# Kernel optimization log

Measured on AMD Instinct MI355X. Metric: run time of the kernel, lower is better.

## Reference

```python
import jax, jax.numpy as jnp
import numpy as np
import math

N = 50000          # nodes
E = 800000         # edges (~avg degree 16)
G = 2048           # graphs
NUM_RBF = 128
CUTOFF = 5.0       # max_radius
C_RAD = 16         # radial channels
SH_DIM = 9         # 1x0e+1x1e+1x2e
_AVG_DEGREE = 15.57930850982666
_AVG_NUM_NODES = 18.03065905448718


def spherical_harmonics_l012(vec):
    """e3nn spherical harmonics l=0,1,2, normalize=True, component normalization."""
    r = jnp.linalg.norm(vec, axis=-1, keepdims=True)
    u = vec / jnp.maximum(r, 1e-12)
    x, y, z = u[..., 0], u[..., 1], u[..., 2]
    s3, s5, s15 = math.sqrt(3.0), math.sqrt(5.0), math.sqrt(15.0)
    x2, y2, z2 = x * x, y * y, z * z
    return jnp.stack([
        jnp.ones_like(x),                 # l=0
        s3 * x, s3 * y, s3 * z,           # l=1
        s15 * x * z,                      # l=2 (e3nn ordering)
        s15 * x * y,
        s5 * (y2 - 0.5 * (x2 + z2)),
        s15 * y * z,
        (s15 / 2.0) * (z2 - x2),
    ], axis=-1)


def exp_normal_smearing(dist):
    """ExpNormalSmearing with cutoff_lower=0, cutoff_upper=CUTOFF, num_rbf=NUM_RBF."""
    alpha = 5.0 / CUTOFF
    start = math.exp(-CUTOFF)
    means = jnp.linspace(start, 1.0, NUM_RBF).astype(dist.dtype)
    beta = (2.0 / NUM_RBF * (1.0 - start)) ** (-2)
    d = dist[..., None]
    cut = 0.5 * (jnp.cos(d * math.pi / CUTOFF) + 1.0) * (d < CUTOFF).astype(d.dtype)
    return cut * jnp.exp(-beta * (jnp.exp(-alpha * d) - means) ** 2)


def setup_inputs() -> dict:
    key = jax.random.key(0)
    ks = jax.random.split(key, 16)
    s = 0.05
    return {
        "pos": jax.random.normal(ks[0], (N, 3), jnp.float32) * 2.0,
        "atom_table": jax.random.normal(ks[1], (64, C_RAD * SH_DIM), jnp.float32) * s,
        "W1": jax.random.normal(ks[2], (NUM_RBF, 64), jnp.float32) * s,
        "b1": jnp.zeros((64,), jnp.float32),
        "W2": jax.random.normal(ks[3], (64, 64), jnp.float32) * s,
        "b2": jnp.zeros((64,), jnp.float32),
        "W3": jax.random.normal(ks[4], (64, C_RAD), jnp.float32) * s,
        "Wh1": jax.random.normal(ks[5], (C_RAD * SH_DIM, C_RAD * SH_DIM), jnp.float32) * s,
        "bh1": jnp.zeros((C_RAD * SH_DIM,), jnp.float32),
        "Wh2": jax.random.normal(ks[6], (C_RAD * SH_DIM, 1), jnp.float32) * s,
        "bh2": jnp.zeros((1,), jnp.float32),
        "node_atom": jax.random.randint(ks[7], (N,), 0, 64, jnp.int32),
        "edge_src": jax.random.randint(ks[8], (E,), 0, N, jnp.int32),
        "edge_dst": jax.random.randint(ks[9], (E,), 0, N, jnp.int32),
        "batch": jnp.sort(jax.random.randint(ks[10], (N,), 0, G, jnp.int32)),
    }


def reference(pos, atom_table, W1, b1, W2, b2, W3, Wh1, bh1, Wh2, bh2,
              node_atom, edge_src, edge_dst, batch):
    # edge geometry
    edge_vec = pos[edge_src] - pos[edge_dst]                      # [E,3]
    edge_len = jnp.linalg.norm(edge_vec, axis=-1)                 # [E]
    rbf = exp_normal_smearing(edge_len)                           # [E,128]
    sh = spherical_harmonics_l012(edge_vec)                       # [E,9]

    # radial MLP (fc_neurons = [128,64,64] -> C_RAD weights)
    h = jax.nn.silu(rbf @ W1 + b1)
    h = jax.nn.silu(h @ W2 + b2)
    rad = h @ W3                                                  # [E,C_RAD]

    # RBF-conditioned tensor-product-style edge message: outer(radial, sh)
    msg = (rad[:, :, None] * sh[:, None, :]).reshape(rad.shape[0], C_RAD * SH_DIM)

    # scatter-add aggregation, rescaled by avg degree (EdgeDegreeEmbedding)
    deg_embed = jax.ops.segment_sum(msg, edge_dst, num_segments=N)
    deg_embed = deg_embed / math.sqrt(_AVG_DEGREE)                # [N,144]

    node_features = atom_table[node_atom] + deg_embed             # [N,144]

    # energy head: Linear -> SiLU -> Linear(1x0e)
    hn = jax.nn.silu(node_features @ Wh1 + bh1)
    node_energy = hn @ Wh2 + bh2                                  # [N,1]

    # ScaledScatter over graphs
    energy = jax.ops.segment_sum(node_energy, batch, num_segments=G)
    energy = energy / math.sqrt(_AVG_NUM_NODES)                   # [G,1]
    return energy
```

## Files before the change

### kernel.cpp

```cpp
#include <hip/hip_runtime.h>
#include <math.h>

#define NND 50000
#define NED 800000
#define NGR 2048
#define NT  1024
#define NB  512
#define NPB 98
#define HALF 49
#define BCAP 2048
#define SCAP 1152
#define LCAP 24
#define LSTR 25
#define BIN_BLOCKS 196
#define TBL_BLOCKS 2

constexpr double dSTART = 0.006737946999085467;
constexpr float  K_START = (float)dSTART;
constexpr float  K_STEP  = (float)((1.0 - dSTART) / 127.0);
constexpr float  K_BETA  = (float)(1.0 / ((2.0/128.0*(1.0-dSTART)) * (2.0/128.0*(1.0-dSTART))));
constexpr float  K_TSTEP = (float)((1.0 - dSTART) / (double)(NT - 1));
constexpr float  K_INVT  = (float)((double)(NT - 1) / (1.0 - dSTART));

__device__ __forceinline__ float silu_f(float x) {
    return x * __builtin_amdgcn_rcpf(1.0f + __expf(-x));
}

__global__ void __launch_bounds__(1024)
bin_table(const int* __restrict__ esrc, const int* __restrict__ edst,
          int* __restrict__ bincnt, unsigned* __restrict__ bins,
          const float* __restrict__ W1, const float* __restrict__ b1,
          const float* __restrict__ W2, const float* __restrict__ b2,
          const float* __restrict__ W3, float* __restrict__ table,
          float* __restrict__ out)
{
    __shared__ unsigned smem[NB + NB * LSTR];
    const int bid = blockIdx.x;
    const int tid = threadIdx.x;

    if (bid < BIN_BLOCKS) {
        int*      lcnt = (int*)smem;
        unsigned* lbuf = smem + NB;
        if (tid < NB) lcnt[tid] = 0;
        __syncthreads();
        const int e0 = bid * 4096;
        #pragma unroll
        for (int r = 0; r < 4; ++r) {
            int e = e0 + r * 1024 + tid;
            if (e < NED) {
                int dst = edst[e];
                int src = esrc[e];
                int b = dst / NPB;
                unsigned rec = ((unsigned)src << 7) | (unsigned)(dst - b * NPB);
                int p = atomicAdd(&lcnt[b], 1);
                if (p < LCAP) lbuf[b * LSTR + p] = rec;
                else {
                    int gp = atomicAdd(&bincnt[b], 1);
                    if (gp < BCAP) bins[b * BCAP + gp] = rec;
                }
            }
        }
        __syncthreads();
        if (tid < NB) {
            int c = lcnt[tid]; c = c < LCAP ? c : LCAP;
            if (c > 0) {
                int base = atomicAdd(&bincnt[tid], c);
                for (int i = 0; i < c; ++i)
                    if (base + i < BCAP) bins[tid * BCAP + base + i] = lbuf[tid * LSTR + i];
            }
        }
        return;
    }

    const int tb = bid - BIN_BLOCKS;
    out[tb * 1024 + tid] = 0.0f;
    if (tid >= 512) return;
    const int ti = tb * 512 + tid;
    const int l  = tid & 63;
    float* hb = (float*)smem + (tid >> 6) * (64 * 17);

    const float xe = K_START + K_TSTEP * (float)ti;
    const float dd = -logf(xe);
    const float cutv = (dd < 5.0f) ? (0.5f * (__cosf(dd * 0.6283185307179586f) + 1.0f)) : 0.0f;

    float h1[64];
    {
        const float4* bp = (const float4*)b1;
        #pragma unroll
        for (int j4 = 0; j4 < 16; ++j4) {
            float4 b = bp[j4];
            h1[4*j4+0] = b.x; h1[4*j4+1] = b.y; h1[4*j4+2] = b.z; h1[4*j4+3] = b.w;
        }
    }
    #pragma unroll 2
    for (int k = 0; k < 128; ++k) {
        float mean = K_START + K_STEP * (float)k;
        float t = xe - mean;
        float rk = cutv * __expf(-K_BETA * t * t);
        const float4* wr = (const float4*)(W1 + (k << 6));
        #pragma unroll
        for (int j4 = 0; j4 < 16; ++j4) {
            float4 wv = wr[j4];
            h1[4*j4+0] = fmaf(rk, wv.x, h1[4*j4+0]);
            h1[4*j4+1] = fmaf(rk, wv.y, h1[4*j4+1]);
            h1[4*j4+2] = fmaf(rk, wv.z, h1[4*j4+2]);
            h1[4*j4+3] = fmaf(rk, wv.w, h1[4*j4+3]);
        }
    }

    float h2[64];
    {
        const float4* bp = (const float4*)b2;
        #pragma unroll
        for (int j4 = 0; j4 < 16; ++j4) {
            float4 b = bp[j4];
            h2[4*j4+0] = b.x; h2[4*j4+1] = b.y; h2[4*j4+2] = b.z; h2[4*j4+3] = b.w;
        }
    }
    #pragma unroll
    for (int ch = 0; ch < 4; ++ch) {
        #pragma unroll
        for (int j = 0; j < 16; ++j) hb[l*17 + j] = silu_f(h1[ch*16 + j]);
        for (int k = 0; k < 16; ++k) {
            float hk = hb[l*17 + k];
            const float4* wr = (const float4*)(W2 + ((ch*16 + k) << 6));
            #pragma unroll
            for (int j4 = 0; j4 < 16; ++j4) {
                float4 wv = wr[j4];
                h2[4*j4+0] = fmaf(hk, wv.x, h2[4*j4+0]);
                h2[4*j4+1] = fmaf(hk, wv.y, h2[4*j4+1]);
                h2[4*j4+2] = fmaf(hk, wv.z, h2[4*j4+2]);
                h2[4*j4+3] = fmaf(hk, wv.w, h2[4*j4+3]);
            }
        }
    }

    float rad[16];
    #pragma unroll
    for (int cc = 0; cc < 16; ++cc) rad[cc] = 0.0f;
    #pragma unroll
    for (int ch = 0; ch < 4; ++ch) {
        #pragma unroll
        for (int j = 0; j < 16; ++j) hb[l*17 + j] = silu_f(h2[ch*16 + j]);
        for (int k = 0; k < 16; ++k) {
            float hk = hb[l*17 + k];
            const float4* wr = (const float4*)(W3 + ((ch*16 + k) << 4));
            #pragma unroll
            for (int c4 = 0; c4 < 4; ++c4) {
                float4 wv = wr[c4];
                rad[4*c4+0] = fmaf(hk, wv.x, rad[4*c4+0]);
                rad[4*c4+1] = fmaf(hk, wv.y, rad[4*c4+1]);
                rad[4*c4+2] = fmaf(hk, wv.z, rad[4*c4+2]);
                rad[4*c4+3] = fmaf(hk, wv.w, rad[4*c4+3]);
            }
        }
    }

    float4* rp = (float4*)(table + (size_t)ti * 16);
    rp[0] = make_float4(rad[0],  rad[1],  rad[2],  rad[3]);
    rp[1] = make_float4(rad[4],  rad[5],  rad[6],  rad[7]);
    rp[2] = make_float4(rad[8],  rad[9],  rad[10], rad[11]);
    rp[3] = make_float4(rad[12], rad[13], rad[14], rad[15]);
}

__global__ void __launch_bounds__(448)
agg_head(const float* __restrict__ pos,
         const int* __restrict__ bincnt, const unsigned* __restrict__ bins,
         const float* __restrict__ table,
         const float* __restrict__ atom_table, const int* __restrict__ node_atom,
         const int* __restrict__ batch,
         const float* __restrict__ Wh1, const float* __restrict__ bh1,
         const float* __restrict__ Wh2, const float* __restrict__ bh2,
         float* __restrict__ out, float isd, float isn)
{
    __shared__ int    lcnt[HALF], soff[HALF], scur[HALF];
    __shared__ float4 sgeo[SCAP];
    __shared__ float  nf_s[7][8][144];
    const int tid = threadIdx.x;
    const int b   = blockIdx.x >> 1;
    const int h   = blockIdx.x & 1;
    const int lbase = h * HALF;
    const int gbase = b * NPB + lbase;

    if (tid < HALF) lcnt[tid] = 0;
    __syncthreads();

    int nrec = bincnt[b]; nrec = nrec < BCAP ? nrec : BCAP;
    const unsigned* myb = bins + b * BCAP;

    for (int i = tid; i < nrec; i += 448) {
        int l = (int)(myb[i] & 127u) - lbase;
        if (l >= 0 && l < HALF) atomicAdd(&lcnt[l], 1);
    }
    __syncthreads();

    if (tid < 64) {
        int v = (tid < HALF) ? lcnt[tid] : 0;
        int x = v;
        #pragma unroll
        for (int off = 1; off < 64; off <<= 1) {
            int u = __shfl_up(x, off);
            if (tid >= off) x += u;
        }
        if (tid < HALF) { soff[tid] = x - v; scur[tid] = x - v; }
    }
    __syncthreads();

    for (int i = tid; i < nrec; i += 448) {
        unsigned rec = myb[i];
        int local = (int)(rec & 127u);
        int l = local - lbase;
        if (l < 0 || l >= HALF) continue;
        int src = (int)(rec >> 7);
        int dst = b * NPB + local;
        float vx = pos[3*src+0] - pos[3*dst+0];
        float vy = pos[3*src+1] - pos[3*dst+1];
        float vz = pos[3*src+2] - pos[3*dst+2];
        float d2 = vx*vx + vy*vy + vz*vz;
        float4 g;
        if (d2 < 25.0f) {
            float ddv = sqrtf(d2);
            float inv = 1.0f / fmaxf(ddv, 1e-12f);
            g = make_float4(vx*inv, vy*inv, vz*inv, __expf(-ddv));
        } else {
            g = make_float4(0.0f, 0.0f, 0.0f, K_START);
        }
        int p = atomicAdd(&scur[l], 1);
        if (p < SCAP) sgeo[p] = g;
    }
    __syncthreads();

    const int lane = tid & 63;
    const int w    = tid >> 6;
    const int g    = lane >> 3;
    const int c    = lane & 7;
    const int l    = w * 8 + g;
    const int gn   = gbase + l;
    const bool valid = (l < HALF) && (gn < NND);

    float acc0[9], acc1[9];
    #pragma unroll
    for (int s = 0; s < 9; ++s) { acc0[s] = 0.0f; acc1[s] = 0.0f; }

    int start = 0, end = 0;
    if (valid) {
        start = soff[l];
        end   = start + lcnt[l];
        end   = end < SCAP ? end : SCAP;
    }

    for (int p = start; p < end; ++p) {
        float4 gv = sgeo[p];
        float ux = gv.x, uy = gv.y, uz = gv.z, xe = gv.w;

        float t = (xe - K_START) * K_INVT;
        int i0 = (int)t;
        i0 = i0 < 0 ? 0 : (i0 > NT-2 ? NT-2 : i0);
        float fr = t - (float)i0;
        const float* tb = table + (size_t)i0 * 16 + c;
        float r0a = tb[0], r1a = tb[16];
        float r0b = tb[8], r1b = tb[24];
        float ra = fmaf(fr, r1a - r0a, r0a);
        float rb = fmaf(fr, r1b - r0b, r0b);

        float sh1 = 1.7320508075688772f * ux;
        float sh2 = 1.7320508075688772f * uy;
        float sh3 = 1.7320508075688772f * uz;
        float sh4 = 3.872983346207417f * ux * uz;
        float sh5 = 3.872983346207417f * ux * uy;
        float sh6 = 2.23606797749979f * (uy*uy - 0.5f*(ux*ux + uz*uz));
        float sh7 = 3.872983346207417f * uy * uz;
        float sh8 = 1.9364916731037085f * (uz*uz - ux*ux);

        acc0[0] += ra;                    acc1[0] += rb;
        acc0[1] = fmaf(ra, sh1, acc0[1]); acc1[1] = fmaf(rb, sh1, acc1[1]);
        acc0[2] = fmaf(ra, sh2, acc0[2]); acc1[2] = fmaf(rb, sh2, acc1[2]);
        acc0[3] = fmaf(ra, sh3, acc0[3]); acc1[3] = fmaf(rb, sh3, acc1[3]);
        acc0[4] = fmaf(ra, sh4, acc0[4]); acc1[4] = fmaf(rb, sh4, acc1[4]);
        acc0[5] = fmaf(ra, sh5, acc0[5]); acc1[5] = fmaf(rb, sh5, acc1[5]);
        acc0[6] = fmaf(ra, sh6, acc0[6]); acc1[6] = fmaf(rb, sh6, acc1[6]);
        acc0[7] = fmaf(ra, sh7, acc0[7]); acc1[7] = fmaf(rb, sh7, acc1[7]);
        acc0[8] = fmaf(ra, sh8, acc0[8]); acc1[8] = fmaf(rb, sh8, acc1[8]);
    }

    {
        int a = valid ? node_atom[gn] : 0;
        const float* at = atom_table + (size_t)a * 144;
        #pragma unroll
        for (int s = 0; s < 9; ++s) {
            nf_s[w][g][c*9 + s]     = fmaf(acc0[s], isd, at[c*9 + s]);
            nf_s[w][g][(c+8)*9 + s] = fmaf(acc1[s], isd, at[(c+8)*9 + s]);
        }
    }

    float A0[8], A1[8], A2[8];
    {
        float bb0 = bh1[lane], bb1 = bh1[lane + 64];
        float bb2 = (lane < 16) ? bh1[lane + 128] : 0.0f;
        #pragma unroll
        for (int q = 0; q < 8; ++q) { A0[q] = bb0; A1[q] = bb1; A2[q] = bb2; }
    }

    for (int k4 = 0; k4 < 36; ++k4) {
        float4 nq[8];
        #pragma unroll
        for (int q = 0; q < 8; ++q)
            nq[q] = *(const float4*)&nf_s[w][q][k4*4];
        const float* wrow = Wh1 + (size_t)(k4*4) * 144;
#define HSTEP(COMP, OFF) { \
        float w0 = wrow[(OFF)*144 + lane]; \
        float w1 = wrow[(OFF)*144 + lane + 64]; \
        float w2 = (lane < 16) ? wrow[(OFF)*144 + lane + 128] : 0.0f; \
        _Pragma("unroll") \
        for (int q = 0; q < 8; ++q) { \
            float nk = nq[q].COMP; \
            A0[q] = fmaf(nk, w0, A0[q]); \
            A1[q] = fmaf(nk, w1, A1[q]); \
            A2[q] = fmaf(nk, w2, A2[q]); } }
        HSTEP(x, 0) HSTEP(y, 1) HSTEP(z, 2) HSTEP(w, 3)
#undef HSTEP
    }

    float wl0 = Wh2[lane], wl1 = Wh2[lane + 64];
    float wl2 = (lane < 16) ? Wh2[lane + 128] : 0.0f;
    float bv  = bh2[0];
    #pragma unroll
    for (int q = 0; q < 8; ++q) {
        float en = silu_f(A0[q]) * wl0 + silu_f(A1[q]) * wl1;
        if (lane < 16) en = fmaf(silu_f(A2[q]), wl2, en);
        en += __shfl_down(en, 32);
        en += __shfl_down(en, 16);
        en += __shfl_down(en, 8);
        en += __shfl_down(en, 4);
        en += __shfl_down(en, 2);
        en += __shfl_down(en, 1);
        int lq = w * 8 + q;
        int gq = gbase + lq;
        if (lane == 0 && lq < HALF && gq < NND) {
            unsafeAtomicAdd(out + batch[gq], (en + bv) * isn);
        }
    }
}

extern "C" void kernel_launch(void* const* d_in, const int* in_sizes, int n_in,
                              void* d_out, int out_size, void* d_ws, size_t ws_size,
                              hipStream_t stream) {
    const float* pos        = (const float*)d_in[0];
    const float* atom_table = (const float*)d_in[1];
    const float* W1         = (const float*)d_in[2];
    const float* b1         = (const float*)d_in[3];
    const float* W2         = (const float*)d_in[4];
    const float* b2         = (const float*)d_in[5];
    const float* W3         = (const float*)d_in[6];
    const float* Wh1        = (const float*)d_in[7];
    const float* bh1        = (const float*)d_in[8];
    const float* Wh2        = (const float*)d_in[9];
    const float* bh2        = (const float*)d_in[10];
    const int*   node_atom  = (const int*)d_in[11];
    const int*   edge_src   = (const int*)d_in[12];
    const int*   edge_dst   = (const int*)d_in[13];
    const int*   batch      = (const int*)d_in[14];

    float* out = (float*)d_out;

    char*     wsb    = (char*)d_ws;
    int*      bincnt = (int*)(wsb);
    float*    table  = (float*)(wsb + 2048);
    unsigned* bins   = (unsigned*)(wsb + 67584);

    hipMemsetAsync(bincnt, 0, NB * 4, stream);

    bin_table<<<BIN_BLOCKS + TBL_BLOCKS, 1024, 0, stream>>>(
        edge_src, edge_dst, bincnt, bins, W1, b1, W2, b2, W3, table, out);

    float isd = 1.0f / sqrtf(15.57930850982666f);
    float isn = 1.0f / sqrtf(18.03065905448718f);
    agg_head<<<NB * 2, 448, 0, stream>>>(
        pos, bincnt, bins, table, atom_table, node_atom, batch,
        Wh1, bh1, Wh2, bh2, out, isd, isn);
}
```

Measured before the change: 239.5 us.

## Replace global atomic bin appends with per-block fixed-slot segments and overflow list

The binning stage no longer does global atomicAdd on per-bin counters. Each of the edge blocks, now twice as many and each covering half as many edges, writes its local LDS buckets into fixed per-(block,bin) slots together with a count array. Rare overflows go to a small global overflow list. The table-building stage is spread over 16 blocks of 64 threads instead of 2 blocks. The aggregation kernel scans all segments for its bin and the overflow list, trading contention-free writes for more strided, sparse reads.

```diff
diff --git a/kernel.cpp b/kernel.cpp
--- a/kernel.cpp
+++ b/kernel.cpp
@@ -8,12 +8,13 @@
 #define NB  512
 #define NPB 98
 #define HALF 49
-#define BCAP 2048
-#define SCAP 1152
+#define EPB 2048
+#define BIN_BLOCKS 391
+#define TBL_BLOCKS 16
 #define LCAP 24
 #define LSTR 25
-#define BIN_BLOCKS 196
-#define TBL_BLOCKS 2
+#define SCAP 1152
+#define OFCAP 256
 
 constexpr double dSTART = 0.006737946999085467;
 constexpr float  K_START = (float)dSTART;
@@ -28,7 +29,8 @@
 
 __global__ void __launch_bounds__(1024)
 bin_table(const int* __restrict__ esrc, const int* __restrict__ edst,
-          int* __restrict__ bincnt, unsigned* __restrict__ bins,
+          unsigned* __restrict__ bins, int* __restrict__ cnts,
+          int* __restrict__ of_cnt, int* __restrict__ of_src, int* __restrict__ of_dst,
           const float* __restrict__ W1, const float* __restrict__ b1,
           const float* __restrict__ W2, const float* __restrict__ b2,
           const float* __restrict__ W3, float* __restrict__ table,
@@ -43,9 +45,9 @@
         unsigned* lbuf = smem + NB;
         if (tid < NB) lcnt[tid] = 0;
         __syncthreads();
-        const int e0 = bid * 4096;
-        #pragma unroll
-        for (int r = 0; r < 4; ++r) {
+        const int e0 = bid * EPB;
+        #pragma unroll
+        for (int r = 0; r < 2; ++r) {
             int e = e0 + r * 1024 + tid;
             if (e < NED) {
                 int dst = edst[e];
@@ -55,29 +57,30 @@
                 int p = atomicAdd(&lcnt[b], 1);
                 if (p < LCAP) lbuf[b * LSTR + p] = rec;
                 else {
-                    int gp = atomicAdd(&bincnt[b], 1);
-                    if (gp < BCAP) bins[b * BCAP + gp] = rec;
+                    int gp = atomicAdd(of_cnt, 1);
+                    if (gp < OFCAP) { of_src[gp] = src; of_dst[gp] = dst; }
                 }
             }
         }
         __syncthreads();
+        unsigned* dp = bins + (size_t)bid * NB * LCAP;
+        for (int i = tid; i < NB * LCAP; i += 1024) {
+            int seg = i / LCAP, k = i - seg * LCAP;
+            dp[i] = lbuf[seg * LSTR + k];
+        }
         if (tid < NB) {
-            int c = lcnt[tid]; c = c < LCAP ? c : LCAP;
-            if (c > 0) {
-                int base = atomicAdd(&bincnt[tid], c);
-                for (int i = 0; i < c; ++i)
-                    if (base + i < BCAP) bins[tid * BCAP + base + i] = lbuf[tid * LSTR + i];
-            }
+            int c = lcnt[tid];
+            cnts[bid * NB + tid] = c < LCAP ? c : LCAP;
         }
         return;
     }
 
     const int tb = bid - BIN_BLOCKS;
-    out[tb * 1024 + tid] = 0.0f;
-    if (tid >= 512) return;
-    const int ti = tb * 512 + tid;
-    const int l  = tid & 63;
-    float* hb = (float*)smem + (tid >> 6) * (64 * 17);
+    if (tid < 128) out[tb * 128 + tid] = 0.0f;
+    if (tid >= 64) return;
+    const int ti = tb * 64 + tid;
+    const int l  = tid;
+    float* hb = (float*)smem;
 
     const float xe = K_START + K_TSTEP * (float)ti;
     const float dd = -logf(xe);
@@ -165,7 +168,9 @@
 
 __global__ void __launch_bounds__(448)
 agg_head(const float* __restrict__ pos,
-         const int* __restrict__ bincnt, const unsigned* __restrict__ bins,
+         const unsigned* __restrict__ bins, const int* __restrict__ cnts,
+         const int* __restrict__ of_cnt, const int* __restrict__ of_src,
+         const int* __restrict__ of_dst,
          const float* __restrict__ table,
          const float* __restrict__ atom_table, const int* __restrict__ node_atom,
          const int* __restrict__ batch,
@@ -174,6 +179,7 @@
          float* __restrict__ out, float isd, float isn)
 {
     __shared__ int    lcnt[HALF], soff[HALF], scur[HALF];
+    __shared__ int    ccache[BIN_BLOCKS];
     __shared__ float4 sgeo[SCAP];
     __shared__ float  nf_s[7][8][144];
     const int tid = threadIdx.x;
@@ -183,13 +189,22 @@
     const int gbase = b * NPB + lbase;
 
     if (tid < HALF) lcnt[tid] = 0;
+    for (int i = tid; i < BIN_BLOCKS; i += 448) ccache[i] = cnts[i * NB + b];
     __syncthreads();
 
-    int nrec = bincnt[b]; nrec = nrec < BCAP ? nrec : BCAP;
-    const unsigned* myb = bins + b * BCAP;
-
-    for (int i = tid; i < nrec; i += 448) {
-        int l = (int)(myb[i] & 127u) - lbase;
+    int ofn = *of_cnt; ofn = ofn < OFCAP ? ofn : OFCAP;
+
+    const int TOT = BIN_BLOCKS * LCAP;
+    for (int s = tid; s < TOT; s += 448) {
+        int seg = s / LCAP, k = s - seg * LCAP;
+        if (k < ccache[seg]) {
+            unsigned rec = bins[((size_t)seg * NB + b) * LCAP + k];
+            int l = (int)(rec & 127u) - lbase;
+            if (l >= 0 && l < HALF) atomicAdd(&lcnt[l], 1);
+        }
+    }
+    for (int i = tid; i < ofn; i += 448) {
+        int l = of_dst[i] - gbase;
         if (l >= 0 && l < HALF) atomicAdd(&lcnt[l], 1);
     }
     __syncthreads();
@@ -206,13 +221,35 @@
     }
     __syncthreads();
 
-    for (int i = tid; i < nrec; i += 448) {
-        unsigned rec = myb[i];
+    for (int s = tid; s < TOT; s += 448) {
+        int seg = s / LCAP, k = s - seg * LCAP;
+        if (k >= ccache[seg]) continue;
+        unsigned rec = bins[((size_t)seg * NB + b) * LCAP + k];
         int local = (int)(rec & 127u);
         int l = local - lbase;
         if (l < 0 || l >= HALF) continue;
         int src = (int)(rec >> 7);
         int dst = b * NPB + local;
+        float vx = pos[3*src+0] - pos[3*dst+0];
+        float vy = pos[3*src+1] - pos[3*dst+1];
+        float vz = pos[3*src+2] - pos[3*dst+2];
+        float d2 = vx*vx + vy*vy + vz*vz;
+        float4 g;
+        if (d2 < 25.0f) {
+            float ddv = sqrtf(d2);
+            float inv = 1.0f / fmaxf(ddv, 1e-12f);
+            g = make_float4(vx*inv, vy*inv, vz*inv, __expf(-ddv));
+        } else {
+            g = make_float4(0.0f, 0.0f, 0.0f, K_START);
+        }
+        int p = atomicAdd(&scur[l], 1);
+        if (p < SCAP) sgeo[p] = g;
+    }
+    for (int i = tid; i < ofn; i += 448) {
+        int dst = of_dst[i];
+        int l = dst - gbase;
+        if (l < 0 || l >= HALF) continue;
+        int src = of_src[i];
         float vx = pos[3*src+0] - pos[3*dst+0];
         float vy = pos[3*src+1] - pos[3*dst+1];
         float vz = pos[3*src+2] - pos[3*dst+2];
@@ -364,18 +401,22 @@
     float* out = (float*)d_out;
 
     char*     wsb    = (char*)d_ws;
-    int*      bincnt = (int*)(wsb);
-    float*    table  = (float*)(wsb + 2048);
-    unsigned* bins   = (unsigned*)(wsb + 67584);
-
-    hipMemsetAsync(bincnt, 0, NB * 4, stream);
+    int*      of_cnt = (int*)(wsb);
+    int*      of_src = (int*)(wsb + 64);
+    int*      of_dst = (int*)(wsb + 1088);
+    float*    table  = (float*)(wsb + 2112);
+    int*      cnts   = (int*)(wsb + 67648);
+    unsigned* bins   = (unsigned*)(wsb + 868416);
+
+    hipMemsetAsync(of_cnt, 0, 4, stream);
 
     bin_table<<<BIN_BLOCKS + TBL_BLOCKS, 1024, 0, stream>>>(
-        edge_src, edge_dst, bincnt, bins, W1, b1, W2, b2, W3, table, out);
+        edge_src, edge_dst, bins, cnts, of_cnt, of_src, of_dst,
+        W1, b1, W2, b2, W3, table, out);
 
     float isd = 1.0f / sqrtf(15.57930850982666f);
     float isn = 1.0f / sqrtf(18.03065905448718f);
     agg_head<<<NB * 2, 448, 0, stream>>>(
-        pos, bincnt, bins, table, atom_table, node_atom, batch,
-        Wh1, bh1, Wh2, bh2, out, isd, isn);
+        pos, bins, cnts, of_cnt, of_src, of_dst, table, atom_table, node_atom,
+        batch, Wh1, bh1, Wh2, bh2, out, isd, isn);
 }
```

Measured after the change: 273.1 us. +14.0%, slower.
